# Optimization experiments

Measured on AMD Instinct MI355X. Metric: run time of the kernel, lower is better.

Reference implementation:

```python
import jax, jax.numpy as jnp
import numpy as np

B, T, L = 256, 2048, 48  # batch, seq_len, nb_labels


def setup_inputs() -> dict:
    key = jax.random.key(0)
    k1, k2, k3 = jax.random.split(key, 3)
    emissions = jax.random.normal(k1, (B, T, L), dtype=jnp.float32)
    tags = jax.random.randint(k2, (B, T), 0, L, dtype=jnp.int32)
    # matches nn.init.uniform_(transitions, -0.1, 0.1)
    transitions = jax.random.uniform(k3, (L, L), dtype=jnp.float32, minval=-0.1, maxval=0.1)
    return {"emissions": emissions, "tags": tags, "transitions": transitions}


def _gold_scores(emissions, tags, transitions):
    # emission score at every gold tag: [B, T] -> sum over T
    e = jnp.take_along_axis(emissions, tags[..., None], axis=2)[..., 0].sum(axis=1)
    # transition scores between consecutive gold tags
    t = transitions[tags[:, :-1], tags[:, 1:]].sum(axis=1)
    start = transitions[0, tags[:, 0]]      # row 0 acts as start scores
    end = transitions[tags[:, -1], -1]      # last column acts as end scores
    return e + t + start + end              # [B]


def _log_partition(emissions, transitions):
    # forward algorithm: alpha_t[b, j] = logsumexp_i(alpha_{t-1}[b, i] + T[i, j]) + em[b, t, j]
    alpha0 = transitions[0][None, :] + emissions[:, 0]          # [B, L]
    em_rest = jnp.moveaxis(emissions[:, 1:], 1, 0)              # [T-1, B, L]

    def step(alpha, em_t):
        alpha = jax.nn.logsumexp(alpha[:, :, None] + transitions[None, :, :], axis=1) + em_t
        return alpha, None

    alpha, _ = jax.lax.scan(step, alpha0, em_rest)
    return jax.nn.logsumexp(alpha + transitions[:, -1][None, :], axis=1)  # [B]


def reference(emissions, tags, transitions):
    """neg_log_likelihood of LinearChainCRF: -sum(scores - log_partition)."""
    scores = _gold_scores(emissions, tags, transitions)
    partition = _log_partition(emissions, transitions)
    return -jnp.sum(scores - partition)
```

## Files before the change

### kernel.cpp

```cpp
#include <hip/hip_runtime.h>

#define B 256
#define T 2048
#define L 48
#define G 8
#define SEG 256
#define KNORM 4.371f
#define TOTALF (B * T * L)

typedef short v4s __attribute__((ext_vector_type(4)));
typedef short v8s __attribute__((ext_vector_type(8)));
typedef float v4f __attribute__((ext_vector_type(4)));
typedef int   v2i __attribute__((ext_vector_type(2)));

#define WAVE_SYNC() asm volatile("s_waitcnt lgkmcnt(0)" ::: "memory")

#if __has_builtin(__builtin_amdgcn_mfma_f32_16x16x16bf16_1k)
#define MFMA16(a, b, c) __builtin_amdgcn_mfma_f32_16x16x16bf16_1k((a), (b), (c), 0, 0, 0)
#else
__device__ __forceinline__ v4f mfma16_asm(v4s a, v4s b, v4f c) {
    asm volatile("v_mfma_f32_16x16x16_bf16 %0, %1, %2, %0\n\ts_nop 7\n\ts_nop 7"
                 : "+v"(c) : "v"(a), "v"(b));
    return c;
}
#define MFMA16(a, b, c) mfma16_asm((a), (b), (c))
#endif

#if __has_builtin(__builtin_amdgcn_mfma_f32_16x16x32_bf16)
typedef __bf16 v8y __attribute__((ext_vector_type(8)));
__device__ __forceinline__ v4f mfma32(v8s a, v8s b, v4f c) {
    return __builtin_amdgcn_mfma_f32_16x16x32_bf16(
        __builtin_bit_cast(v8y, a), __builtin_bit_cast(v8y, b), c, 0, 0, 0);
}
#else
__device__ __forceinline__ v4f mfma32(v8s a, v8s b, v4f c) {
    asm volatile("v_mfma_f32_16x16x32_bf16 %0, %1, %2, %0\n\ts_nop 7\n\ts_nop 7"
                 : "+v"(c) : "v"(a), "v"(b));
    return c;
}
#endif

__device__ __forceinline__ unsigned cvt_pk(float lo, float hi) {
    unsigned r;
    asm("v_cvt_pk_bf16_f32 %0, %1, %2" : "=v"(r) : "v"(lo), "v"(hi));
    return r;
}

__device__ __forceinline__ v4s scale_pack(v4f cf, v4f g) {
    v4f a = cf * g;
    v2i d;
    d.x = (int)cvt_pk(a.x, a.y);
    d.y = (int)cvt_pk(a.z, a.w);
    return __builtin_bit_cast(v4s, d);
}

__device__ __forceinline__ v8s fuse01(v4s n0, v4s n1) {
    v2i a_ = __builtin_bit_cast(v2i, n0);
    v2i b_ = __builtin_bit_cast(v2i, n1);
    int4 fw; fw.x = a_.x; fw.y = a_.y; fw.z = b_.x; fw.w = b_.y;
    return __builtin_bit_cast(v8s, fw);
}

__global__ __launch_bounds__(192, 6) void crf_scan(
    const float* __restrict__ em, const int* __restrict__ tags,
    const float* __restrict__ trans, float* __restrict__ out,
    float* __restrict__ ws)
{
    const int b   = blockIdx.x >> 3;
    const int s   = blockIdx.x & 7;
    const int tid = threadIdx.x;
    const int ct  = tid >> 6;
    const int ln  = tid & 63;
    const int q   = ln >> 4;
    const int c   = ln & 15;

    __shared__ __align__(16) float smem[2 * 384];

    const size_t bem = (size_t)b * T * L;
    const int t0 = 1 + SEG * s;
    const int t1 = (t0 + SEG < T) ? (t0 + SEG) : T;

    v8s A32[3];
    #pragma unroll
    for (int rt = 0; rt < 3; ++rt) {
        const int m = 16 * rt + c;
        uint4 aw;
        aw.x = cvt_pk(__expf(trans[(4 * q + 0) * L + m]),
                      __expf(trans[(4 * q + 1) * L + m]));
        aw.y = cvt_pk(__expf(trans[(4 * q + 2) * L + m]),
                      __expf(trans[(4 * q + 3) * L + m]));
        aw.z = cvt_pk(__expf(trans[(16 + 4 * q + 0) * L + m]),
                      __expf(trans[(16 + 4 * q + 1) * L + m]));
        aw.w = cvt_pk(__expf(trans[(16 + 4 * q + 2) * L + m]),
                      __expf(trans[(16 + 4 * q + 3) * L + m]));
        A32[rt] = __builtin_bit_cast(v8s, aw);
    }
    v4s A16[3];
    #pragma unroll
    for (int rt = 0; rt < 3; ++rt) {
        const int m = 16 * rt + c;
        v2i d;
        d.x = (int)cvt_pk(__expf(trans[(32 + 4 * q + 0) * L + m]),
                          __expf(trans[(32 + 4 * q + 1) * L + m]));
        d.y = (int)cvt_pk(__expf(trans[(32 + 4 * q + 2) * L + m]),
                          __expf(trans[(32 + 4 * q + 3) * L + m]));
        A16[rt] = __builtin_bit_cast(v4s, d);
    }

    const int col = 16 * ct + c;
    v8s Bq01;
    v4s Bq2;
    {
        int4 w;
        w.x = (4 * q + 0 == col ? 0x3F80 : 0) | (4 * q + 1 == col ? 0x3F800000 : 0);
        w.y = (4 * q + 2 == col ? 0x3F80 : 0) | (4 * q + 3 == col ? 0x3F800000 : 0);
        w.z = (16 + 4 * q + 0 == col ? 0x3F80 : 0) | (16 + 4 * q + 1 == col ? 0x3F800000 : 0);
        w.w = (16 + 4 * q + 2 == col ? 0x3F80 : 0) | (16 + 4 * q + 3 == col ? 0x3F800000 : 0);
        Bq01 = __builtin_bit_cast(v8s, w);
        v2i d2;
        d2.x = (32 + 4 * q + 0 == col ? 0x3F80 : 0) | (32 + 4 * q + 1 == col ? 0x3F800000 : 0);
        d2.y = (32 + 4 * q + 2 == col ? 0x3F80 : 0) | (32 + 4 * q + 3 == col ? 0x3F800000 : 0);
        Bq2 = __builtin_bit_cast(v4s, d2);
    }

    const v4f zero4 = {0.f, 0.f, 0.f, 0.f};

    auto do_step = [&](const float* rowp) {
        v4f gv0 = *(const v4f*)(rowp + 4 * q);
        v4f gv1 = *(const v4f*)(rowp + 16 + 4 * q);
        v4f gv2 = *(const v4f*)(rowp + 32 + 4 * q);
        v4f Cf0, Cf1, Cf2;
        {
            v4f acc = mfma32(A32[0], Bq01, zero4);
            Cf0 = MFMA16(A16[0], Bq2, acc);
        }
        {
            v4f acc = mfma32(A32[1], Bq01, zero4);
            Cf1 = MFMA16(A16[1], Bq2, acc);
        }
        {
            v4f acc = mfma32(A32[2], Bq01, zero4);
            Cf2 = MFMA16(A16[2], Bq2, acc);
        }
        v4s n0 = scale_pack(Cf0, gv0);
        v4s n1 = scale_pack(Cf1, gv1);
        Bq01 = fuse01(n0, n1);
        Bq2  = scale_pack(Cf2, gv2);
    };

    {
        size_t gf = bem + (size_t)t0 * L;
        smem[tid]       = __expf(em[gf + tid]       - KNORM);
        smem[tid + 192] = __expf(em[gf + tid + 192] - KNORM);
        __syncthreads();
    }

    for (int bk = 0; bk < SEG / 8; ++bk) {
        const float* cur = smem + (bk & 1) * 384;
        float* nxt = smem + ((bk & 1) ^ 1) * 384;

        size_t gf = bem + (size_t)(t0 + 8 * (bk + 1)) * L;
        if (gf > (size_t)TOTALF - 384) gf = (size_t)TOTALF - 384;
        float stg0 = em[gf + tid];
        float stg1 = em[gf + tid + 192];

        #pragma unroll
        for (int k = 0; k < 8; ++k)
            if (t0 + 8 * bk + k < t1)
                do_step(cur + 48 * k);

        nxt[tid]       = __expf(stg0 - KNORM);
        nxt[tid + 192] = __expf(stg1 - KNORM);
        __syncthreads();
    }

    unsigned short* qs = (unsigned short*)ws + (size_t)(b * G + s) * 2304;
    v2i dt[3];
    {
        int4 w01 = __builtin_bit_cast(int4, Bq01);
        dt[0].x = w01.x; dt[0].y = w01.y;
        dt[1].x = w01.z; dt[1].y = w01.w;
        dt[2] = __builtin_bit_cast(v2i, Bq2);
    }
    #pragma unroll
    for (int kt = 0; kt < 3; ++kt) {
        v2i d = dt[kt];
        int r0 = 16 * kt + 4 * q;
        qs[(r0 + 0) * 48 + col] = (unsigned short)((unsigned)d.x & 0xffffu);
        qs[(r0 + 1) * 48 + col] = (unsigned short)((unsigned)d.x >> 16);
        qs[(r0 + 2) * 48 + col] = (unsigned short)((unsigned)d.y & 0xffffu);
        qs[(r0 + 3) * 48 + col] = (unsigned short)((unsigned)d.y >> 16);
    }

    const int* tg = tags + (size_t)b * T;
    float gp = 0.f;
    if (tid < 128) {
        #pragma unroll
        for (int j = 0; j < 2; ++j) {
            int t = SEG * s + 128 * j + tid;
            int tag = tg[t];
            gp += em[bem + (size_t)t * L + tag];
            if (t < T - 1)  gp += trans[tag * L + tg[t + 1]];
            if (t == 0)     gp += trans[tag];
            if (t == T - 1) gp += trans[tag * L + (L - 1)];
        }
    }
    #pragma unroll
    for (int off = 32; off; off >>= 1) gp += __shfl_xor(gp, off);
    __shared__ float red[3];
    if (ln == 0) red[ct] = gp;
    __syncthreads();
    if (tid == 0) atomicAdd(out, -(red[0] + red[1] + red[2]));
}

__global__ __launch_bounds__(64) void crf_combine(
    const float* __restrict__ em, const float* __restrict__ trans,
    const float* __restrict__ ws, float* __restrict__ out)
{
    const int b = blockIdx.x, l = threadIdx.x;
    const int lc = (l < L) ? l : (L - 1);

    __shared__ float us[64];

    const unsigned short* qb = (const unsigned short*)ws + (size_t)b * G * 2304;

    float u = (l < L) ? __expf(trans[l] + em[(size_t)b * T * L + l]) : 0.f;
    float logtot = 2047.0f * KNORM;

    uint4 pre[6];
    {
        const uint4* p = (const uint4*)(qb + lc * 48);
        #pragma unroll
        for (int ii = 0; ii < 6; ++ii) pre[ii] = p[ii];
    }

    for (int s = 0; s < G; ++s) {
        us[l] = u;
        uint4 cur[6];
        #pragma unroll
        for (int ii = 0; ii < 6; ++ii) cur[ii] = pre[ii];
        if (s + 1 < G) {
            const uint4* p = (const uint4*)(qb + (size_t)(s + 1) * 2304 + lc * 48);
            #pragma unroll
            for (int ii = 0; ii < 6; ++ii) pre[ii] = p[ii];
        }
        WAVE_SYNC();

        float acc = 0.f;
        #pragma unroll
        for (int ii = 0; ii < 6; ++ii) {
            unsigned w0 = cur[ii].x, w1 = cur[ii].y, w2 = cur[ii].z, w3 = cur[ii].w;
            int jj = ii * 8;
            acc = fmaf(__uint_as_float(w0 << 16),          us[jj + 0], acc);
            acc = fmaf(__uint_as_float(w0 & 0xffff0000u),  us[jj + 1], acc);
            acc = fmaf(__uint_as_float(w1 << 16),          us[jj + 2], acc);
            acc = fmaf(__uint_as_float(w1 & 0xffff0000u),  us[jj + 3], acc);
            acc = fmaf(__uint_as_float(w2 << 16),          us[jj + 4], acc);
            acc = fmaf(__uint_as_float(w2 & 0xffff0000u),  us[jj + 5], acc);
            acc = fmaf(__uint_as_float(w3 << 16),          us[jj + 6], acc);
            acc = fmaf(__uint_as_float(w3 & 0xffff0000u),  us[jj + 7], acc);
        }
        WAVE_SYNC();

        float r = __int_as_float(
            __builtin_amdgcn_readlane(__float_as_int(acc), 0));
        logtot += __logf(r);
        u = (l < L) ? acc * __builtin_amdgcn_rcpf(r) : 0.f;
    }

    float v = (l < L) ? u * __expf(trans[lc * L + (L - 1)]) : 0.f;
    #pragma unroll
    for (int off = 32; off; off >>= 1) v += __shfl_xor(v, off);
    if (l == 0) atomicAdd(out, logtot + __logf(v));
}

extern "C" void kernel_launch(void* const* d_in, const int* in_sizes, int n_in,
                              void* d_out, int out_size, void* d_ws, size_t ws_size,
                              hipStream_t stream) {
    const float* em    = (const float*)d_in[0];
    const int*   tags  = (const int*)  d_in[1];
    const float* trans = (const float*)d_in[2];
    float* out = (float*)d_out;
    float* ws  = (float*)d_ws;

    (void)hipMemsetAsync(out, 0, sizeof(float), stream);
    crf_scan   <<<B * G, 192, 0, stream>>>(em, tags, trans, out, ws);
    crf_combine<<<B,      64, 0, stream>>>(em, trans, ws, out);
}
```

Baseline: 266.6 us.

## Split scan into single-wave blocks per column tile and halve segment length

Each 192-thread block that handled one (batch, segment) is replaced by three independent 64-thread blocks, one per 16-column tile. Every block now stages the full emission tile itself and uses a wave-local LDS wait instead of block barriers. Segments shrink from 256 to 128 steps, doubling the number of segments so the serial chain per block is shorter and more blocks run concurrently. The cost is three-fold redundant emission loads and exp work per segment, plus a larger combine stage over 16 segment matrices.

```diff
diff --git a/kernel.cpp b/kernel.cpp
--- a/kernel.cpp
+++ b/kernel.cpp
@@ -3,8 +3,8 @@
 #define B 256
 #define T 2048
 #define L 48
-#define G 8
-#define SEG 256
+#define G 16
+#define SEG 128
 #define KNORM 4.371f
 #define TOTALF (B * T * L)
 
@@ -61,16 +61,17 @@
     return __builtin_bit_cast(v8s, fw);
 }
 
-__global__ __launch_bounds__(192, 6) void crf_scan(
+__global__ __launch_bounds__(64) void crf_scan(
     const float* __restrict__ em, const int* __restrict__ tags,
     const float* __restrict__ trans, float* __restrict__ out,
     float* __restrict__ ws)
 {
-    const int b   = blockIdx.x >> 3;
-    const int s   = blockIdx.x & 7;
-    const int tid = threadIdx.x;
-    const int ct  = tid >> 6;
-    const int ln  = tid & 63;
+    const int idx = blockIdx.x;
+    const int ct  = idx % 3;
+    const int bs  = idx / 3;
+    const int s   = bs & 15;
+    const int b   = bs >> 4;
+    const int ln  = threadIdx.x;
     const int q   = ln >> 4;
     const int c   = ln & 15;
 
@@ -150,28 +151,31 @@
 
     {
         size_t gf = bem + (size_t)t0 * L;
-        smem[tid]       = __expf(em[gf + tid]       - KNORM);
-        smem[tid + 192] = __expf(em[gf + tid + 192] - KNORM);
-        __syncthreads();
-    }
-
-    for (int bk = 0; bk < SEG / 8; ++bk) {
+        #pragma unroll
+        for (int j = 0; j < 6; ++j)
+            smem[ln + 64 * j] = __expf(em[gf + ln + 64 * j] - KNORM);
+        WAVE_SYNC();
+    }
+
+    for (int bk = 0; bk < 16; ++bk) {
         const float* cur = smem + (bk & 1) * 384;
         float* nxt = smem + ((bk & 1) ^ 1) * 384;
 
         size_t gf = bem + (size_t)(t0 + 8 * (bk + 1)) * L;
         if (gf > (size_t)TOTALF - 384) gf = (size_t)TOTALF - 384;
-        float stg0 = em[gf + tid];
-        float stg1 = em[gf + tid + 192];
+        float stg[6];
+        #pragma unroll
+        for (int j = 0; j < 6; ++j) stg[j] = em[gf + ln + 64 * j];
 
         #pragma unroll
         for (int k = 0; k < 8; ++k)
             if (t0 + 8 * bk + k < t1)
                 do_step(cur + 48 * k);
 
-        nxt[tid]       = __expf(stg0 - KNORM);
-        nxt[tid + 192] = __expf(stg1 - KNORM);
-        __syncthreads();
+        #pragma unroll
+        for (int j = 0; j < 6; ++j)
+            nxt[ln + 64 * j] = __expf(stg[j] - KNORM);
+        WAVE_SYNC();
     }
 
     unsigned short* qs = (unsigned short*)ws + (size_t)(b * G + s) * 2304;
@@ -192,25 +196,22 @@
         qs[(r0 + 3) * 48 + col] = (unsigned short)((unsigned)d.y >> 16);
     }
 
-    const int* tg = tags + (size_t)b * T;
-    float gp = 0.f;
-    if (tid < 128) {
+    if (ct == 0) {
+        const int* tg = tags + (size_t)b * T;
+        float gp = 0.f;
         #pragma unroll
         for (int j = 0; j < 2; ++j) {
-            int t = SEG * s + 128 * j + tid;
+            int t = SEG * s + 64 * j + ln;
             int tag = tg[t];
             gp += em[bem + (size_t)t * L + tag];
             if (t < T - 1)  gp += trans[tag * L + tg[t + 1]];
             if (t == 0)     gp += trans[tag];
             if (t == T - 1) gp += trans[tag * L + (L - 1)];
         }
-    }
-    #pragma unroll
-    for (int off = 32; off; off >>= 1) gp += __shfl_xor(gp, off);
-    __shared__ float red[3];
-    if (ln == 0) red[ct] = gp;
-    __syncthreads();
-    if (tid == 0) atomicAdd(out, -(red[0] + red[1] + red[2]));
+        #pragma unroll
+        for (int off = 32; off; off >>= 1) gp += __shfl_xor(gp, off);
+        if (ln == 0) atomicAdd(out, -gp);
+    }
 }
 
 __global__ __launch_bounds__(64) void crf_combine(
@@ -284,6 +285,6 @@
     float* ws  = (float*)d_ws;
 
     (void)hipMemsetAsync(out, 0, sizeof(float), stream);
-    crf_scan   <<<B * G, 192, 0, stream>>>(em, tags, trans, out, ws);
-    crf_combine<<<B,      64, 0, stream>>>(em, trans, ws, out);
-}
+    crf_scan   <<<B * G * 3, 64, 0, stream>>>(em, tags, trans, out, ws);
+    crf_combine<<<B,         64, 0, stream>>>(em, trans, ws, out);
+}
```

Result: slower. 281.8 us (+5.7%).
